# Kernel tuning notes

Measured on AMD Instinct MI355X. Metric: run time of the kernel, lower is better.

## Reference

```python
import jax, jax.numpy as jnp
import numpy as np

K_NEIGHBORS = 5
EPS = 1e-12  # torch F.normalize eps


def _l2_normalize(x):
    n = jnp.linalg.norm(x, axis=-1, keepdims=True)
    return x / jnp.maximum(n, EPS)


def setup_inputs() -> dict:
    key = jax.random.key(0)
    k1, k2, k3, k4 = jax.random.split(key, 4)
    B, D = 256, 512
    N, A = 50000, 8
    return {
        "z_flowed": jax.random.normal(k1, (B, D), dtype=jnp.float32),
        "target_attrs": jax.random.randint(k2, (B, A), 0, 3, dtype=jnp.int32),
        "train_embeddings": jax.random.normal(k3, (N, D), dtype=jnp.float32),
        "train_attributes": jax.random.randint(k4, (N, A), 0, 3, dtype=jnp.int32),
    }


def reference(z_flowed, target_attrs, train_embeddings, train_attributes):
    B = z_flowed.shape[0]
    A = target_attrs.shape[1]
    z_norm = _l2_normalize(z_flowed)          # [B, D]
    train_norm = _l2_normalize(train_embeddings)  # [N, D]

    # batched attribute match: [B, N] count of matching attributes
    match_score = (train_attributes[None, :, :] == target_attrs[:, None, :]).sum(-1)
    mask = (match_score >= (A - 1)).astype(z_norm.dtype)  # [B, N]

    # cosine similarities for all samples in one GEMM: [B, N]
    sims = jnp.einsum('nd,bd->bn', train_norm, z_norm)
    masked_sim = sims * mask

    top_k_values, _ = jax.lax.top_k(masked_sim, K_NEIGHBORS)  # [B, K]
    per_sample_loss = (1.0 - top_k_values).mean(-1)           # [B]

    # samples with fewer than k matching neighbors are skipped in the sum
    valid = (mask.sum(-1) >= K_NEIGHBORS).astype(per_sample_loss.dtype)
    return (per_sample_loss * valid).sum() / B
```

## Files before the change

kernel.cpp:

```cpp
#include <hip/hip_runtime.h>
#include <math.h>


constexpr int D = 512;
constexpr int A = 8;
constexpr int K_NEI = 5;
constexpr int SLOTS = 512;
constexpr int CSTRIDE = 16;
constexpr int PAIR_CAP = 65536;
constexpr int LDS_PAIR_CAP = 1024;
constexpr int DOT_BLOCKS = 2304;

__device__ __forceinline__ float wave_reduce_add(float v) {
    #pragma unroll
    for (int m = 1; m < 64; m <<= 1) v += __shfl_xor(v, m, 64);
    return v;
}

__global__ __launch_bounds__(64) void prep_kernel(
    const float* __restrict__ z, const int* __restrict__ tattr,
    float* __restrict__ z_norm, unsigned* __restrict__ tpacked,
    int* __restrict__ counters, int* __restrict__ npairs,
    float* __restrict__ out)
{
    const int b = blockIdx.x;
    const int lane = threadIdx.x;
    const float4* zrow = (const float4*)(z + (size_t)b * D);
    float4 v0 = zrow[lane * 2 + 0];
    float4 v1 = zrow[lane * 2 + 1];
    float ss = v0.x*v0.x + v0.y*v0.y + v0.z*v0.z + v0.w*v0.w
             + v1.x*v1.x + v1.y*v1.y + v1.z*v1.z + v1.w*v1.w;
    ss = wave_reduce_add(ss);
    const float scale = 1.0f / fmaxf(sqrtf(ss), 1e-12f);
    v0.x *= scale; v0.y *= scale; v0.z *= scale; v0.w *= scale;
    v1.x *= scale; v1.y *= scale; v1.z *= scale; v1.w *= scale;
    float4* orow = (float4*)(z_norm + (size_t)b * D);
    orow[lane * 2 + 0] = v0;
    orow[lane * 2 + 1] = v1;
    if (lane == 0) {
        unsigned p = 0;
        #pragma unroll
        for (int a = 0; a < A; a++)
            p |= ((unsigned)tattr[b * A + a] & 0xFu) << (4 * a);
        tpacked[b] = p;
        counters[b * CSTRIDE] = 0;
        if (b == 0) { *npairs = 0; out[0] = 0.0f; }
    }
}

__global__ __launch_bounds__(256) void match_kernel(
    const int* __restrict__ trattr, const unsigned* __restrict__ tpacked,
    unsigned* __restrict__ pairs, int* __restrict__ npairs, int N)
{
    __shared__ unsigned s_tp[256];
    __shared__ unsigned s_pairs[LDS_PAIR_CAP];
    __shared__ int s_cnt, s_base;

    const int tid = threadIdx.x;
    const int n = blockIdx.x * 256 + tid;
    s_tp[tid] = tpacked[tid];
    if (tid == 0) s_cnt = 0;
    __syncthreads();

    if (n < N) {
        const int4* a4 = (const int4*)(trattr + (size_t)n * A);
        const int4 x = a4[0], y = a4[1];
        const unsigned p =
             ((unsigned)x.x & 0xFu)        | (((unsigned)x.y & 0xFu) << 4)
           | (((unsigned)x.z & 0xFu) << 8)  | (((unsigned)x.w & 0xFu) << 12)
           | (((unsigned)y.x & 0xFu) << 16) | (((unsigned)y.y & 0xFu) << 20)
           | (((unsigned)y.z & 0xFu) << 24) | (((unsigned)y.w & 0xFu) << 28);

        const uint4* tp4 = (const uint4*)s_tp;
        #pragma unroll 4
        for (int bq = 0; bq < 64; bq++) {
            const uint4 t = tp4[bq];
            #pragma unroll
            for (int j = 0; j < 4; j++) {
                const unsigned tv = (j == 0) ? t.x : (j == 1) ? t.y : (j == 2) ? t.z : t.w;
                const unsigned yv = p ^ tv;
                const unsigned nzhi = ((((yv & 0x77777777u) + 0x77777777u) | yv) & 0x88888888u);
                if (__popc(nzhi) <= 1) {
                    const int idx = atomicAdd(&s_cnt, 1);
                    if (idx < LDS_PAIR_CAP)
                        s_pairs[idx] = ((unsigned)n << 8) | (unsigned)(bq * 4 + j);
                }
            }
        }
    }
    __syncthreads();
    const int cnt = min(s_cnt, LDS_PAIR_CAP);
    if (tid == 0) s_base = atomicAdd(npairs, cnt);
    __syncthreads();
    const int base = s_base;
    for (int i = tid; i < cnt; i += 256)
        if (base + i < PAIR_CAP) pairs[base + i] = s_pairs[i];
}

__global__ __launch_bounds__(256) void dot_kernel(
    const float* __restrict__ train, const float* __restrict__ z_norm,
    const unsigned* __restrict__ pairs, const int* __restrict__ npairs,
    int* __restrict__ counters, float* __restrict__ simbuf)
{
    const int lane = threadIdx.x & 15;
    const int g0 = blockIdx.x * 16 + (threadIdx.x >> 4);
    const int ngroups = DOT_BLOCKS * 16;
    const int np = min(*npairs, PAIR_CAP);

    for (int i = g0; i < np; i += ngroups) {
        const unsigned pr = pairs[i];
        const float4* __restrict__ row4 = (const float4*)(train  + (size_t)(pr >> 8)   * D);
        const float4* __restrict__ zr4  = (const float4*)(z_norm + (size_t)(pr & 255u) * D);

        float4 r[8], zz[8];
        #pragma unroll
        for (int j = 0; j < 8; j++) r[j]  = row4[j * 16 + lane];
        #pragma unroll
        for (int j = 0; j < 8; j++) zz[j] = zr4[j * 16 + lane];

        float ss = 0.0f, dd = 0.0f;
        #pragma unroll
        for (int j = 0; j < 8; j++) {
            ss += r[j].x*r[j].x  + r[j].y*r[j].y  + r[j].z*r[j].z  + r[j].w*r[j].w;
            dd += r[j].x*zz[j].x + r[j].y*zz[j].y + r[j].z*zz[j].z + r[j].w*zz[j].w;
        }
        #pragma unroll
        for (int m = 1; m < 16; m <<= 1) {
            ss += __shfl_xor(ss, m, 64);
            dd += __shfl_xor(dd, m, 64);
        }
        if (lane == 0) {
            const int b = (int)(pr & 255u);
            const float sim = dd / fmaxf(sqrtf(ss), 1e-12f);
            const int idx = atomicAdd(&counters[b * CSTRIDE], 1);
            if (idx < SLOTS) simbuf[(size_t)b * SLOTS + idx] = sim;
        }
    }
}

__global__ __launch_bounds__(64) void topk_kernel(
    const int* __restrict__ counters, const float* __restrict__ simbuf,
    float* __restrict__ out, int Bt)
{
    const int b = blockIdx.x;
    const int lane = threadIdx.x;
    const int cnt = counters[b * CSTRIDE];
    const int m = min(cnt, SLOTS);
    const float* buf = simbuf + (size_t)b * SLOTS;

    float v[8];
    #pragma unroll
    for (int k = 0; k < 8; k++) {
        const int i = lane + k * 64;
        v[k] = (i < m) ? buf[i] : -1e30f;
    }

    float s = 0.0f;
    #pragma unroll
    for (int r = 0; r < K_NEI; r++) {
        float best = v[0];
        #pragma unroll
        for (int k = 1; k < 8; k++) best = fmaxf(best, v[k]);
        float M = best;
        #pragma unroll
        for (int mm = 1; mm < 64; mm <<= 1) M = fmaxf(M, __shfl_xor(M, mm, 64));
        s += fmaxf(M, 0.0f);
        const unsigned long long bal = __ballot(best == M);
        const int first = __ffsll(bal) - 1;
        if (lane == first) {
            if      (v[0] == M) v[0] = -1e30f;
            else if (v[1] == M) v[1] = -1e30f;
            else if (v[2] == M) v[2] = -1e30f;
            else if (v[3] == M) v[3] = -1e30f;
            else if (v[4] == M) v[4] = -1e30f;
            else if (v[5] == M) v[5] = -1e30f;
            else if (v[6] == M) v[6] = -1e30f;
            else                v[7] = -1e30f;
        }
    }

    if (lane == 0) {
        const float contrib = (cnt >= K_NEI) ? (1.0f - s * (1.0f / K_NEI)) : 0.0f;
        atomicAdd(out, contrib / (float)Bt);
    }
}

extern "C" void kernel_launch(void* const* d_in, const int* in_sizes, int n_in,
                              void* d_out, int out_size, void* d_ws, size_t ws_size,
                              hipStream_t stream)
{
    const float* z      = (const float*)d_in[0];
    const int*   tattr  = (const int*)d_in[1];
    const float* train  = (const float*)d_in[2];
    const int*   trattr = (const int*)d_in[3];
    float* out = (float*)d_out;

    const int B = in_sizes[0] / D;
    const int N = in_sizes[2] / D;

    char* ws = (char*)d_ws;
    float*    z_norm   = (float*)ws;    ws += (size_t)B * D * sizeof(float);
    unsigned* tpacked  = (unsigned*)ws; ws += (size_t)B * sizeof(unsigned);
    int*      counters = (int*)ws;      ws += (size_t)B * CSTRIDE * sizeof(int);
    float*    simbuf   = (float*)ws;    ws += (size_t)B * SLOTS * sizeof(float);
    int*      npairs   = (int*)ws;      ws += 64;
    unsigned* pairs    = (unsigned*)ws;

    prep_kernel<<<B, 64, 0, stream>>>(z, tattr, z_norm, tpacked, counters, npairs, out);
    match_kernel<<<(N + 255) / 256, 256, 0, stream>>>(trattr, tpacked, pairs, npairs, N);
    dot_kernel<<<DOT_BLOCKS, 256, 0, stream>>>(train, z_norm, pairs, npairs, counters, simbuf);
    topk_kernel<<<B, 64, 0, stream>>>(counters, simbuf, out, B);
}
```

Baseline: 176.4 us.

## Bucket matches per query and fuse dot products with top-k per query block

The global pair list is replaced with per-query buckets filled through global atomics in the match kernel. Dot products and top-k are fused into one 1024-thread block per query that keeps similarities in shared memory. Query normalization and attribute packing move into the consumer kernels, which drops the prep kernel and the separate top-k launch. This removes one launch and the simbuf round trip, but it adds contended global atomics on 256 counters and limits the dot phase to 256 blocks.

```diff
diff --git a/kernel.cpp b/kernel.cpp
--- a/kernel.cpp
+++ b/kernel.cpp
@@ -7,69 +7,40 @@
 constexpr int K_NEI = 5;
 constexpr int SLOTS = 512;
 constexpr int CSTRIDE = 16;
-constexpr int PAIR_CAP = 65536;
-constexpr int LDS_PAIR_CAP = 1024;
-constexpr int DOT_BLOCKS = 2304;
 
-__device__ __forceinline__ float wave_reduce_add(float v) {
-    #pragma unroll
-    for (int m = 1; m < 64; m <<= 1) v += __shfl_xor(v, m, 64);
-    return v;
+__device__ __forceinline__ unsigned pack_attrs(const int4 x, const int4 y) {
+    return  ((unsigned)x.x & 0xFu)        | (((unsigned)x.y & 0xFu) << 4)
+          | (((unsigned)x.z & 0xFu) << 8)  | (((unsigned)x.w & 0xFu) << 12)
+          | (((unsigned)y.x & 0xFu) << 16) | (((unsigned)y.y & 0xFu) << 20)
+          | (((unsigned)y.z & 0xFu) << 24) | (((unsigned)y.w & 0xFu) << 28);
 }
 
-__global__ __launch_bounds__(64) void prep_kernel(
-    const float* __restrict__ z, const int* __restrict__ tattr,
-    float* __restrict__ z_norm, unsigned* __restrict__ tpacked,
-    int* __restrict__ counters, int* __restrict__ npairs,
-    float* __restrict__ out)
+__global__ __launch_bounds__(256) void zero_kernel(
+    int* __restrict__ counters, float* __restrict__ out, int total)
 {
-    const int b = blockIdx.x;
-    const int lane = threadIdx.x;
-    const float4* zrow = (const float4*)(z + (size_t)b * D);
-    float4 v0 = zrow[lane * 2 + 0];
-    float4 v1 = zrow[lane * 2 + 1];
-    float ss = v0.x*v0.x + v0.y*v0.y + v0.z*v0.z + v0.w*v0.w
-             + v1.x*v1.x + v1.y*v1.y + v1.z*v1.z + v1.w*v1.w;
-    ss = wave_reduce_add(ss);
-    const float scale = 1.0f / fmaxf(sqrtf(ss), 1e-12f);
-    v0.x *= scale; v0.y *= scale; v0.z *= scale; v0.w *= scale;
-    v1.x *= scale; v1.y *= scale; v1.z *= scale; v1.w *= scale;
-    float4* orow = (float4*)(z_norm + (size_t)b * D);
-    orow[lane * 2 + 0] = v0;
-    orow[lane * 2 + 1] = v1;
-    if (lane == 0) {
-        unsigned p = 0;
-        #pragma unroll
-        for (int a = 0; a < A; a++)
-            p |= ((unsigned)tattr[b * A + a] & 0xFu) << (4 * a);
-        tpacked[b] = p;
-        counters[b * CSTRIDE] = 0;
-        if (b == 0) { *npairs = 0; out[0] = 0.0f; }
-    }
+    const int i = blockIdx.x * 256 + threadIdx.x;
+    if (i < total) counters[i] = 0;
+    if (i == 0) out[0] = 0.0f;
 }
 
 __global__ __launch_bounds__(256) void match_kernel(
-    const int* __restrict__ trattr, const unsigned* __restrict__ tpacked,
-    unsigned* __restrict__ pairs, int* __restrict__ npairs, int N)
+    const int* __restrict__ trattr, const int* __restrict__ tattr,
+    unsigned* __restrict__ bucket, int* __restrict__ counters, int N)
 {
     __shared__ unsigned s_tp[256];
-    __shared__ unsigned s_pairs[LDS_PAIR_CAP];
-    __shared__ int s_cnt, s_base;
 
     const int tid = threadIdx.x;
     const int n = blockIdx.x * 256 + tid;
-    s_tp[tid] = tpacked[tid];
-    if (tid == 0) s_cnt = 0;
+
+    {
+        const int4* t4 = (const int4*)(tattr + (size_t)tid * A);
+        s_tp[tid] = pack_attrs(t4[0], t4[1]);
+    }
     __syncthreads();
 
     if (n < N) {
         const int4* a4 = (const int4*)(trattr + (size_t)n * A);
-        const int4 x = a4[0], y = a4[1];
-        const unsigned p =
-             ((unsigned)x.x & 0xFu)        | (((unsigned)x.y & 0xFu) << 4)
-           | (((unsigned)x.z & 0xFu) << 8)  | (((unsigned)x.w & 0xFu) << 12)
-           | (((unsigned)y.x & 0xFu) << 16) | (((unsigned)y.y & 0xFu) << 20)
-           | (((unsigned)y.z & 0xFu) << 24) | (((unsigned)y.w & 0xFu) << 28);
+        const unsigned p = pack_attrs(a4[0], a4[1]);
 
         const uint4* tp4 = (const uint4*)s_tp;
         #pragma unroll 4
@@ -81,42 +52,53 @@
                 const unsigned yv = p ^ tv;
                 const unsigned nzhi = ((((yv & 0x77777777u) + 0x77777777u) | yv) & 0x88888888u);
                 if (__popc(nzhi) <= 1) {
-                    const int idx = atomicAdd(&s_cnt, 1);
-                    if (idx < LDS_PAIR_CAP)
-                        s_pairs[idx] = ((unsigned)n << 8) | (unsigned)(bq * 4 + j);
+                    const int b = bq * 4 + j;
+                    const int idx = atomicAdd(&counters[b * CSTRIDE], 1);
+                    if (idx < SLOTS) bucket[(size_t)b * SLOTS + idx] = (unsigned)n;
                 }
             }
         }
     }
-    __syncthreads();
-    const int cnt = min(s_cnt, LDS_PAIR_CAP);
-    if (tid == 0) s_base = atomicAdd(npairs, cnt);
-    __syncthreads();
-    const int base = s_base;
-    for (int i = tid; i < cnt; i += 256)
-        if (base + i < PAIR_CAP) pairs[base + i] = s_pairs[i];
 }
 
-__global__ __launch_bounds__(256) void dot_kernel(
-    const float* __restrict__ train, const float* __restrict__ z_norm,
-    const unsigned* __restrict__ pairs, const int* __restrict__ npairs,
-    int* __restrict__ counters, float* __restrict__ simbuf)
+__global__ __launch_bounds__(1024) void dot_topk_kernel(
+    const float* __restrict__ train, const float* __restrict__ z,
+    const unsigned* __restrict__ bucket, const int* __restrict__ counters,
+    float* __restrict__ out, int Bt)
 {
-    const int lane = threadIdx.x & 15;
-    const int g0 = blockIdx.x * 16 + (threadIdx.x >> 4);
-    const int ngroups = DOT_BLOCKS * 16;
-    const int np = min(*npairs, PAIR_CAP);
+    __shared__ float s_sims[SLOTS];
 
-    for (int i = g0; i < np; i += ngroups) {
-        const unsigned pr = pairs[i];
-        const float4* __restrict__ row4 = (const float4*)(train  + (size_t)(pr >> 8)   * D);
-        const float4* __restrict__ zr4  = (const float4*)(z_norm + (size_t)(pr & 255u) * D);
+    const int b = blockIdx.x;
+    const int tid = threadIdx.x;
+    const int lane = tid & 15;
+    const int grp = tid >> 4;
+    constexpr int NGRP = 64;
 
-        float4 r[8], zz[8];
+    const float4* z4 = (const float4*)(z + (size_t)b * D);
+    float4 zz[8];
+    #pragma unroll
+    for (int j = 0; j < 8; j++) zz[j] = z4[j * 16 + lane];
+    float zs = 0.0f;
+    #pragma unroll
+    for (int j = 0; j < 8; j++)
+        zs += zz[j].x*zz[j].x + zz[j].y*zz[j].y + zz[j].z*zz[j].z + zz[j].w*zz[j].w;
+    #pragma unroll
+    for (int m = 1; m < 16; m <<= 1) zs += __shfl_xor(zs, m, 64);
+    const float zscale = 1.0f / fmaxf(sqrtf(zs), 1e-12f);
+    #pragma unroll
+    for (int j = 0; j < 8; j++) {
+        zz[j].x *= zscale; zz[j].y *= zscale; zz[j].z *= zscale; zz[j].w *= zscale;
+    }
+
+    const int cnt = counters[b * CSTRIDE];
+    const int m = min(cnt, SLOTS);
+
+    for (int i = grp; i < m; i += NGRP) {
+        const int n = (int)bucket[(size_t)b * SLOTS + i];
+        const float4* __restrict__ row4 = (const float4*)(train + (size_t)n * D);
+        float4 r[8];
         #pragma unroll
-        for (int j = 0; j < 8; j++) r[j]  = row4[j * 16 + lane];
-        #pragma unroll
-        for (int j = 0; j < 8; j++) zz[j] = zr4[j * 16 + lane];
+        for (int j = 0; j < 8; j++) r[j] = row4[j * 16 + lane];
 
         float ss = 0.0f, dd = 0.0f;
         #pragma unroll
@@ -125,63 +107,50 @@
             dd += r[j].x*zz[j].x + r[j].y*zz[j].y + r[j].z*zz[j].z + r[j].w*zz[j].w;
         }
         #pragma unroll
-        for (int m = 1; m < 16; m <<= 1) {
-            ss += __shfl_xor(ss, m, 64);
-            dd += __shfl_xor(dd, m, 64);
+        for (int mm = 1; mm < 16; mm <<= 1) {
+            ss += __shfl_xor(ss, mm, 64);
+            dd += __shfl_xor(dd, mm, 64);
         }
-        if (lane == 0) {
-            const int b = (int)(pr & 255u);
-            const float sim = dd / fmaxf(sqrtf(ss), 1e-12f);
-            const int idx = atomicAdd(&counters[b * CSTRIDE], 1);
-            if (idx < SLOTS) simbuf[(size_t)b * SLOTS + idx] = sim;
+        if (lane == 0) s_sims[i] = dd / fmaxf(sqrtf(ss), 1e-12f);
+    }
+    __syncthreads();
+
+    if (tid < 64) {
+        float v[8];
+        #pragma unroll
+        for (int k = 0; k < 8; k++) {
+            const int i = tid + k * 64;
+            v[k] = (i < m) ? s_sims[i] : -1e30f;
         }
-    }
-}
 
-__global__ __launch_bounds__(64) void topk_kernel(
-    const int* __restrict__ counters, const float* __restrict__ simbuf,
-    float* __restrict__ out, int Bt)
-{
-    const int b = blockIdx.x;
-    const int lane = threadIdx.x;
-    const int cnt = counters[b * CSTRIDE];
-    const int m = min(cnt, SLOTS);
-    const float* buf = simbuf + (size_t)b * SLOTS;
+        float s = 0.0f;
+        #pragma unroll
+        for (int r = 0; r < K_NEI; r++) {
+            float best = v[0];
+            #pragma unroll
+            for (int k = 1; k < 8; k++) best = fmaxf(best, v[k]);
+            float M = best;
+            #pragma unroll
+            for (int mm = 1; mm < 64; mm <<= 1) M = fmaxf(M, __shfl_xor(M, mm, 64));
+            s += fmaxf(M, 0.0f);
+            const unsigned long long bal = __ballot(best == M);
+            const int first = __ffsll(bal) - 1;
+            if (tid == first) {
+                if      (v[0] == M) v[0] = -1e30f;
+                else if (v[1] == M) v[1] = -1e30f;
+                else if (v[2] == M) v[2] = -1e30f;
+                else if (v[3] == M) v[3] = -1e30f;
+                else if (v[4] == M) v[4] = -1e30f;
+                else if (v[5] == M) v[5] = -1e30f;
+                else if (v[6] == M) v[6] = -1e30f;
+                else                v[7] = -1e30f;
+            }
+        }
 
-    float v[8];
-    #pragma unroll
-    for (int k = 0; k < 8; k++) {
-        const int i = lane + k * 64;
-        v[k] = (i < m) ? buf[i] : -1e30f;
-    }
-
-    float s = 0.0f;
-    #pragma unroll
-    for (int r = 0; r < K_NEI; r++) {
-        float best = v[0];
-        #pragma unroll
-        for (int k = 1; k < 8; k++) best = fmaxf(best, v[k]);
-        float M = best;
-        #pragma unroll
-        for (int mm = 1; mm < 64; mm <<= 1) M = fmaxf(M, __shfl_xor(M, mm, 64));
-        s += fmaxf(M, 0.0f);
-        const unsigned long long bal = __ballot(best == M);
-        const int first = __ffsll(bal) - 1;
-        if (lane == first) {
-            if      (v[0] == M) v[0] = -1e30f;
-            else if (v[1] == M) v[1] = -1e30f;
-            else if (v[2] == M) v[2] = -1e30f;
-            else if (v[3] == M) v[3] = -1e30f;
-            else if (v[4] == M) v[4] = -1e30f;
-            else if (v[5] == M) v[5] = -1e30f;
-            else if (v[6] == M) v[6] = -1e30f;
-            else                v[7] = -1e30f;
+        if (tid == 0) {
+            const float contrib = (cnt >= K_NEI) ? (1.0f - s * (1.0f / K_NEI)) : 0.0f;
+            atomicAdd(out, contrib / (float)Bt);
         }
-    }
-
-    if (lane == 0) {
-        const float contrib = (cnt >= K_NEI) ? (1.0f - s * (1.0f / K_NEI)) : 0.0f;
-        atomicAdd(out, contrib / (float)Bt);
     }
 }
 
@@ -199,15 +168,11 @@
     const int N = in_sizes[2] / D;
 
     char* ws = (char*)d_ws;
-    float*    z_norm   = (float*)ws;    ws += (size_t)B * D * sizeof(float);
-    unsigned* tpacked  = (unsigned*)ws; ws += (size_t)B * sizeof(unsigned);
     int*      counters = (int*)ws;      ws += (size_t)B * CSTRIDE * sizeof(int);
-    float*    simbuf   = (float*)ws;    ws += (size_t)B * SLOTS * sizeof(float);
-    int*      npairs   = (int*)ws;      ws += 64;
-    unsigned* pairs    = (unsigned*)ws;
+    unsigned* bucket   = (unsigned*)ws; ws += (size_t)B * SLOTS * sizeof(unsigned);
 
-    prep_kernel<<<B, 64, 0, stream>>>(z, tattr, z_norm, tpacked, counters, npairs, out);
-    match_kernel<<<(N + 255) / 256, 256, 0, stream>>>(trattr, tpacked, pairs, npairs, N);
-    dot_kernel<<<DOT_BLOCKS, 256, 0, stream>>>(train, z_norm, pairs, npairs, counters, simbuf);
-    topk_kernel<<<B, 64, 0, stream>>>(counters, simbuf, out, B);
+    const int ctotal = B * CSTRIDE;
+    zero_kernel<<<(ctotal + 255) / 256, 256, 0, stream>>>(counters, out, ctotal);
+    match_kernel<<<(N + 255) / 256, 256, 0, stream>>>(trattr, tattr, bucket, counters, N);
+    dot_topk_kernel<<<B, 1024, 0, stream>>>(train, z, bucket, counters, out, B);
 }
```

New measurement: 186.8 us. +5.9%, slower.

## Fuse top-k into dot kernel via last-arriver counters and drop z_norm materialization

Applied to the files above, without the earlier changes.

The separate top-k kernel is removed. Each query's top-5 is now computed inside the dot kernel by whichever 16-lane group finishes the final similarity for that query, detected with per-query expected and done counters. The prep kernel now stores only inverse norms, so no normalized z buffer is written, and packing of target attributes moves into the match kernel. The match loop start is also rotated per row to spread the per-query atomic increments. This saves one launch and a buffer round trip, at the cost of a global atomic per match in the match kernel and a serialized 16-lane top-k scan over up to 512 values on the last-arriving group.

```diff
diff --git a/kernel.cpp b/kernel.cpp
--- a/kernel.cpp
+++ b/kernel.cpp
@@ -11,46 +11,40 @@
 constexpr int LDS_PAIR_CAP = 1024;
 constexpr int DOT_BLOCKS = 2304;
 
-__device__ __forceinline__ float wave_reduce_add(float v) {
-    #pragma unroll
-    for (int m = 1; m < 64; m <<= 1) v += __shfl_xor(v, m, 64);
-    return v;
+__device__ __forceinline__ unsigned pack_attrs(const int4 x, const int4 y) {
+    return  ((unsigned)x.x & 0xFu)        | (((unsigned)x.y & 0xFu) << 4)
+          | (((unsigned)x.z & 0xFu) << 8)  | (((unsigned)x.w & 0xFu) << 12)
+          | (((unsigned)y.x & 0xFu) << 16) | (((unsigned)y.y & 0xFu) << 20)
+          | (((unsigned)y.z & 0xFu) << 24) | (((unsigned)y.w & 0xFu) << 28);
 }
 
 __global__ __launch_bounds__(64) void prep_kernel(
-    const float* __restrict__ z, const int* __restrict__ tattr,
-    float* __restrict__ z_norm, unsigned* __restrict__ tpacked,
-    int* __restrict__ counters, int* __restrict__ npairs,
-    float* __restrict__ out)
+    const float* __restrict__ z, float* __restrict__ zinv,
+    int* __restrict__ counters, int* __restrict__ expected,
+    int* __restrict__ done, int* __restrict__ npairs, float* __restrict__ out)
 {
     const int b = blockIdx.x;
     const int lane = threadIdx.x;
     const float4* zrow = (const float4*)(z + (size_t)b * D);
-    float4 v0 = zrow[lane * 2 + 0];
-    float4 v1 = zrow[lane * 2 + 1];
+    const float4 v0 = zrow[lane * 2 + 0];
+    const float4 v1 = zrow[lane * 2 + 1];
     float ss = v0.x*v0.x + v0.y*v0.y + v0.z*v0.z + v0.w*v0.w
              + v1.x*v1.x + v1.y*v1.y + v1.z*v1.z + v1.w*v1.w;
-    ss = wave_reduce_add(ss);
-    const float scale = 1.0f / fmaxf(sqrtf(ss), 1e-12f);
-    v0.x *= scale; v0.y *= scale; v0.z *= scale; v0.w *= scale;
-    v1.x *= scale; v1.y *= scale; v1.z *= scale; v1.w *= scale;
-    float4* orow = (float4*)(z_norm + (size_t)b * D);
-    orow[lane * 2 + 0] = v0;
-    orow[lane * 2 + 1] = v1;
+    #pragma unroll
+    for (int m = 1; m < 64; m <<= 1) ss += __shfl_xor(ss, m, 64);
     if (lane == 0) {
-        unsigned p = 0;
-        #pragma unroll
-        for (int a = 0; a < A; a++)
-            p |= ((unsigned)tattr[b * A + a] & 0xFu) << (4 * a);
-        tpacked[b] = p;
+        zinv[b] = 1.0f / fmaxf(sqrtf(ss), 1e-12f);
         counters[b * CSTRIDE] = 0;
+        expected[b * CSTRIDE] = 0;
+        done[b * CSTRIDE]     = 0;
         if (b == 0) { *npairs = 0; out[0] = 0.0f; }
     }
 }
 
 __global__ __launch_bounds__(256) void match_kernel(
-    const int* __restrict__ trattr, const unsigned* __restrict__ tpacked,
-    unsigned* __restrict__ pairs, int* __restrict__ npairs, int N)
+    const int* __restrict__ trattr, const int* __restrict__ tattr,
+    unsigned* __restrict__ pairs, int* __restrict__ npairs,
+    int* __restrict__ expected, int N)
 {
     __shared__ unsigned s_tp[256];
     __shared__ unsigned s_pairs[LDS_PAIR_CAP];
@@ -58,22 +52,22 @@
 
     const int tid = threadIdx.x;
     const int n = blockIdx.x * 256 + tid;
-    s_tp[tid] = tpacked[tid];
+
+    {
+        const int4* t4 = (const int4*)(tattr + (size_t)tid * A);
+        s_tp[tid] = pack_attrs(t4[0], t4[1]);
+    }
     if (tid == 0) s_cnt = 0;
     __syncthreads();
 
     if (n < N) {
         const int4* a4 = (const int4*)(trattr + (size_t)n * A);
-        const int4 x = a4[0], y = a4[1];
-        const unsigned p =
-             ((unsigned)x.x & 0xFu)        | (((unsigned)x.y & 0xFu) << 4)
-           | (((unsigned)x.z & 0xFu) << 8)  | (((unsigned)x.w & 0xFu) << 12)
-           | (((unsigned)y.x & 0xFu) << 16) | (((unsigned)y.y & 0xFu) << 20)
-           | (((unsigned)y.z & 0xFu) << 24) | (((unsigned)y.w & 0xFu) << 28);
-
+        const unsigned p = pack_attrs(a4[0], a4[1]);
         const uint4* tp4 = (const uint4*)s_tp;
+        const int start = n & 63;
         #pragma unroll 4
-        for (int bq = 0; bq < 64; bq++) {
+        for (int bqi = 0; bqi < 64; bqi++) {
+            const int bq = (start + bqi) & 63;
             const uint4 t = tp4[bq];
             #pragma unroll
             for (int j = 0; j < 4; j++) {
@@ -81,9 +75,11 @@
                 const unsigned yv = p ^ tv;
                 const unsigned nzhi = ((((yv & 0x77777777u) + 0x77777777u) | yv) & 0x88888888u);
                 if (__popc(nzhi) <= 1) {
+                    const int b = bq * 4 + j;
+                    atomicAdd(&expected[b * CSTRIDE], 1);
                     const int idx = atomicAdd(&s_cnt, 1);
                     if (idx < LDS_PAIR_CAP)
-                        s_pairs[idx] = ((unsigned)n << 8) | (unsigned)(bq * 4 + j);
+                        s_pairs[idx] = ((unsigned)n << 8) | (unsigned)b;
                 }
             }
         }
@@ -97,91 +93,104 @@
         if (base + i < PAIR_CAP) pairs[base + i] = s_pairs[i];
 }
 
-__global__ __launch_bounds__(256) void dot_kernel(
-    const float* __restrict__ train, const float* __restrict__ z_norm,
-    const unsigned* __restrict__ pairs, const int* __restrict__ npairs,
-    int* __restrict__ counters, float* __restrict__ simbuf)
+__global__ __launch_bounds__(256) void dot_topk_kernel(
+    const float* __restrict__ train, const float* __restrict__ z,
+    const float* __restrict__ zinv, const unsigned* __restrict__ pairs,
+    const int* __restrict__ npairs, int* __restrict__ counters,
+    const int* __restrict__ expected, int* __restrict__ done,
+    float* __restrict__ simbuf, float* __restrict__ out, int Bt)
 {
     const int lane = threadIdx.x & 15;
     const int g0 = blockIdx.x * 16 + (threadIdx.x >> 4);
     const int ngroups = DOT_BLOCKS * 16;
     const int np = min(*npairs, PAIR_CAP);
+    const int lw = threadIdx.x & 63;
+    const int gbase = lw & ~15;
+    const unsigned long long gmask = 0xFFFFull << gbase;
 
     for (int i = g0; i < np; i += ngroups) {
         const unsigned pr = pairs[i];
-        const float4* __restrict__ row4 = (const float4*)(train  + (size_t)(pr >> 8)   * D);
-        const float4* __restrict__ zr4  = (const float4*)(z_norm + (size_t)(pr & 255u) * D);
-
-        float4 r[8], zz[8];
-        #pragma unroll
-        for (int j = 0; j < 8; j++) r[j]  = row4[j * 16 + lane];
-        #pragma unroll
-        for (int j = 0; j < 8; j++) zz[j] = zr4[j * 16 + lane];
+        const int n = (int)(pr >> 8);
+        const int b = (int)(pr & 255u);
+        const float4* __restrict__ row4 = (const float4*)(train + (size_t)n * D);
+        const float4* __restrict__ z4   = (const float4*)(z     + (size_t)b * D);
+
+        float4 r[8], q[8];
+        #pragma unroll
+        for (int j = 0; j < 8; j++) r[j] = row4[j * 16 + lane];
+        #pragma unroll
+        for (int j = 0; j < 8; j++) q[j] = z4[j * 16 + lane];
+        const float zi = zinv[b];
+        #pragma unroll
+        for (int j = 0; j < 8; j++) {
+            q[j].x *= zi; q[j].y *= zi; q[j].z *= zi; q[j].w *= zi;
+        }
 
         float ss = 0.0f, dd = 0.0f;
         #pragma unroll
         for (int j = 0; j < 8; j++) {
-            ss += r[j].x*r[j].x  + r[j].y*r[j].y  + r[j].z*r[j].z  + r[j].w*r[j].w;
-            dd += r[j].x*zz[j].x + r[j].y*zz[j].y + r[j].z*zz[j].z + r[j].w*zz[j].w;
-        }
-        #pragma unroll
-        for (int m = 1; m < 16; m <<= 1) {
-            ss += __shfl_xor(ss, m, 64);
-            dd += __shfl_xor(dd, m, 64);
-        }
+            ss += r[j].x*r[j].x + r[j].y*r[j].y + r[j].z*r[j].z + r[j].w*r[j].w;
+            dd += r[j].x*q[j].x + r[j].y*q[j].y + r[j].z*q[j].z + r[j].w*q[j].w;
+        }
+        #pragma unroll
+        for (int mm = 1; mm < 16; mm <<= 1) {
+            ss += __shfl_xor(ss, mm, 64);
+            dd += __shfl_xor(dd, mm, 64);
+        }
+
+        int lastf = 0;
         if (lane == 0) {
-            const int b = (int)(pr & 255u);
             const float sim = dd / fmaxf(sqrtf(ss), 1e-12f);
             const int idx = atomicAdd(&counters[b * CSTRIDE], 1);
-            if (idx < SLOTS) simbuf[(size_t)b * SLOTS + idx] = sim;
-        }
-    }
-}
-
-__global__ __launch_bounds__(64) void topk_kernel(
-    const int* __restrict__ counters, const float* __restrict__ simbuf,
-    float* __restrict__ out, int Bt)
-{
-    const int b = blockIdx.x;
-    const int lane = threadIdx.x;
-    const int cnt = counters[b * CSTRIDE];
-    const int m = min(cnt, SLOTS);
-    const float* buf = simbuf + (size_t)b * SLOTS;
-
-    float v[8];
-    #pragma unroll
-    for (int k = 0; k < 8; k++) {
-        const int i = lane + k * 64;
-        v[k] = (i < m) ? buf[i] : -1e30f;
-    }
-
-    float s = 0.0f;
-    #pragma unroll
-    for (int r = 0; r < K_NEI; r++) {
-        float best = v[0];
-        #pragma unroll
-        for (int k = 1; k < 8; k++) best = fmaxf(best, v[k]);
-        float M = best;
-        #pragma unroll
-        for (int mm = 1; mm < 64; mm <<= 1) M = fmaxf(M, __shfl_xor(M, mm, 64));
-        s += fmaxf(M, 0.0f);
-        const unsigned long long bal = __ballot(best == M);
-        const int first = __ffsll(bal) - 1;
-        if (lane == first) {
-            if      (v[0] == M) v[0] = -1e30f;
-            else if (v[1] == M) v[1] = -1e30f;
-            else if (v[2] == M) v[2] = -1e30f;
-            else if (v[3] == M) v[3] = -1e30f;
-            else if (v[4] == M) v[4] = -1e30f;
-            else if (v[5] == M) v[5] = -1e30f;
-            else if (v[6] == M) v[6] = -1e30f;
-            else                v[7] = -1e30f;
-        }
-    }
-
-    if (lane == 0) {
-        const float contrib = (cnt >= K_NEI) ? (1.0f - s * (1.0f / K_NEI)) : 0.0f;
-        atomicAdd(out, contrib / (float)Bt);
+            if (idx < SLOTS)
+                __hip_atomic_store(&simbuf[(size_t)b * SLOTS + idx], sim,
+                                   __ATOMIC_RELAXED, __HIP_MEMORY_SCOPE_AGENT);
+            const int d = __hip_atomic_fetch_add(&done[b * CSTRIDE], 1,
+                                   __ATOMIC_ACQ_REL, __HIP_MEMORY_SCOPE_AGENT);
+            lastf = (d == expected[b * CSTRIDE] - 1);
+        }
+        lastf = __shfl(lastf, gbase, 64);
+
+        if (lastf) {
+            __threadfence();
+            const int totc = expected[b * CSTRIDE];
+            const int m = min(totc, SLOTS);
+            const float* buf = simbuf + (size_t)b * SLOTS;
+
+            float v[32];
+            #pragma unroll
+            for (int k = 0; k < 32; k++) {
+                const int s_i = k * 16 + lane;
+                v[k] = (s_i < m)
+                     ? __hip_atomic_load(&buf[s_i], __ATOMIC_RELAXED,
+                                         __HIP_MEMORY_SCOPE_AGENT)
+                     : -1e30f;
+            }
+
+            float s = 0.0f;
+            #pragma unroll
+            for (int r5 = 0; r5 < K_NEI; r5++) {
+                float best = v[0];
+                #pragma unroll
+                for (int k = 1; k < 32; k++) best = fmaxf(best, v[k]);
+                float M = best;
+                #pragma unroll
+                for (int mm = 1; mm < 16; mm <<= 1) M = fmaxf(M, __shfl_xor(M, mm, 64));
+                s += fmaxf(M, 0.0f);
+                const unsigned long long bal = __ballot(best == M) & gmask;
+                const int first = __ffsll(bal) - 1;
+                if (lw == first) {
+                    #pragma unroll
+                    for (int k = 0; k < 32; k++) {
+                        if (v[k] == M) { v[k] = -1e30f; break; }
+                    }
+                }
+            }
+            if (lane == 0) {
+                const float contrib = (totc >= K_NEI) ? (1.0f - s * (1.0f / K_NEI)) : 0.0f;
+                atomicAdd(out, contrib / (float)Bt);
+            }
+        }
     }
 }
 
@@ -199,15 +208,16 @@
     const int N = in_sizes[2] / D;
 
     char* ws = (char*)d_ws;
-    float*    z_norm   = (float*)ws;    ws += (size_t)B * D * sizeof(float);
-    unsigned* tpacked  = (unsigned*)ws; ws += (size_t)B * sizeof(unsigned);
+    float*    zinv     = (float*)ws;    ws += (size_t)B * sizeof(float);
     int*      counters = (int*)ws;      ws += (size_t)B * CSTRIDE * sizeof(int);
+    int*      expected = (int*)ws;      ws += (size_t)B * CSTRIDE * sizeof(int);
+    int*      done     = (int*)ws;      ws += (size_t)B * CSTRIDE * sizeof(int);
     float*    simbuf   = (float*)ws;    ws += (size_t)B * SLOTS * sizeof(float);
     int*      npairs   = (int*)ws;      ws += 64;
     unsigned* pairs    = (unsigned*)ws;
 
-    prep_kernel<<<B, 64, 0, stream>>>(z, tattr, z_norm, tpacked, counters, npairs, out);
-    match_kernel<<<(N + 255) / 256, 256, 0, stream>>>(trattr, tpacked, pairs, npairs, N);
-    dot_kernel<<<DOT_BLOCKS, 256, 0, stream>>>(train, z_norm, pairs, npairs, counters, simbuf);
-    topk_kernel<<<B, 64, 0, stream>>>(counters, simbuf, out, B);
-}
+    prep_kernel<<<B, 64, 0, stream>>>(z, zinv, counters, expected, done, npairs, out);
+    match_kernel<<<(N + 255) / 256, 256, 0, stream>>>(trattr, tattr, pairs, npairs, expected, N);
+    dot_topk_kernel<<<DOT_BLOCKS, 256, 0, stream>>>(train, z, zinv, pairs, npairs,
+                                                    counters, expected, done, simbuf, out, B);
+}
```

New measurement: 385.7 us. 119% more time.
